# Kernel tuning notes

Hardware: AMD Instinct MI355X
Metric: run time of the kernel (lower is better)

## Reference

```python
import jax, jax.numpy as jnp
import numpy as np

EPS = 1e-5
GROUPS = 32


def _groupnorm(x, gamma, beta):
    B, C, H, W = x.shape
    xr = x.reshape(B, GROUPS, C // GROUPS, H, W)
    mu = xr.mean(axis=(2, 3, 4), keepdims=True)
    var = xr.var(axis=(2, 3, 4), keepdims=True)
    xn = ((xr - mu) * jax.lax.rsqrt(var + EPS)).reshape(B, C, H, W)
    return xn * gamma[None, :, None, None] + beta[None, :, None, None]


def _conv1x1(x, w, b):
    # x: [B,C,H,W], w: [Cout,Cin], b: [Cout]
    return jnp.einsum('bchw,oc->bohw', x, w) + b[None, :, None, None]


def setup_inputs() -> dict:
    key = jax.random.key(0)
    ks = jax.random.split(key, 11)
    B, C, H, W = 4, 64, 64, 64
    s = 0.05  # weight scale for well-conditioned softmax
    inp = {
        'x': jax.random.normal(ks[0], (B, C, H, W), jnp.float32),
        'gn_gamma': jnp.ones((C,), jnp.float32),
        'gn_beta': jnp.zeros((C,), jnp.float32),
        'wq': jax.random.normal(ks[1], (C, C), jnp.float32) * s,
        'bq': jnp.zeros((C,), jnp.float32),
        'wk': jax.random.normal(ks[2], (C, C), jnp.float32) * s,
        'bk': jnp.zeros((C,), jnp.float32),
        'wv': jax.random.normal(ks[3], (C, C), jnp.float32) * s,
        'bv': jnp.zeros((C,), jnp.float32),
        'wp': jax.random.normal(ks[4], (C, C), jnp.float32) * s,
        'bp': jnp.zeros((C,), jnp.float32),
    }
    return inp


def reference(x, gn_gamma, gn_beta, wq, bq, wk, bk, wv, bv, wp, bp):
    B, C, H, W = x.shape
    h = _groupnorm(x, gn_gamma, gn_beta)
    q = _conv1x1(h, wq, bq)
    k = _conv1x1(h, wk, bk)
    v = _conv1x1(h, wv, bv)
    # scores over all spatial positions: [B,H,W,H,W]
    scale = 1.0 / jnp.sqrt(jnp.asarray(C, x.dtype))
    w = jnp.einsum('bchw,bcHW->bhwHW', q, k) * scale
    w = jax.nn.softmax(w.reshape(B, H, W, H * W), axis=-1).reshape(B, H, W, H, W)
    h = jnp.einsum('bhwHW,bcHW->bchw', w, v)
    h = _conv1x1(h, wp, bp)
    return x + h
```

## Files before the change

### kernel.cpp

```cpp
#include <hip/hip_runtime.h>
#include <stdint.h>

#define Bn 4
#define Cn 64
#define Sn 4096
#define Gn 32

typedef float v4f __attribute__((ext_vector_type(4)));
typedef short v8s __attribute__((ext_vector_type(8)));
typedef short v4s __attribute__((ext_vector_type(4)));

#define MFMA16(a,b,c) __builtin_amdgcn_mfma_f32_16x16x32_bf16((a),(b),(c),0,0,0)

__device__ __forceinline__ float bf2f(uint16_t u){
  union { uint32_t i; float f; } x; x.i = ((uint32_t)u) << 16; return x.f;
}
__device__ __forceinline__ uint16_t f2bf(float f){
  union { float f; uint32_t i; } x; x.f = f;
  uint32_t r = x.i + 0x7fffu + ((x.i >> 16) & 1u);
  return (uint16_t)(r >> 16);
}
__device__ __forceinline__ uint16_t f2bf_trunc(float f){
  union { float f; uint32_t i; } x; x.f = f;
  return (uint16_t)(x.i >> 16);
}
__device__ __forceinline__ v8s pack8(float4 a, float4 b){
  v8s r;
  r[0]=(short)f2bf(a.x); r[1]=(short)f2bf(a.y); r[2]=(short)f2bf(a.z); r[3]=(short)f2bf(a.w);
  r[4]=(short)f2bf(b.x); r[5]=(short)f2bf(b.y); r[6]=(short)f2bf(b.z); r[7]=(short)f2bf(b.w);
  return r;
}

__global__ __launch_bounds__(256) void gn_stats(const float* __restrict__ x,
                                                float* __restrict__ stats)
{
  const int tid = threadIdx.x;
  const float* base = x + (size_t)blockIdx.x * 8192;
  float sum = 0.f, sq = 0.f;
  #pragma unroll
  for (int i = 0; i < 8; ++i) {
    float4 v = *(const float4*)(base + ((i << 8) + tid)*4);
    sum += v.x + v.y + v.z + v.w;
    sq  += v.x*v.x + v.y*v.y + v.z*v.z + v.w*v.w;
  }
  #pragma unroll
  for (int off = 1; off < 64; off <<= 1) {
    sum += __shfl_xor(sum, off);
    sq  += __shfl_xor(sq, off);
  }
  __shared__ float red[8];
  const int w = tid >> 6;
  if ((tid & 63) == 0) { red[w] = sum; red[4+w] = sq; }
  __syncthreads();
  if (tid == 0) {
    float s = red[0]+red[1]+red[2]+red[3];
    float q = red[4]+red[5]+red[6]+red[7];
    float mean = s * (1.f/8192.f);
    float var  = q * (1.f/8192.f) - mean*mean;
    stats[blockIdx.x]       = mean;
    stats[128 + blockIdx.x] = rsqrtf(fmaxf(var, 0.f) + 1e-5f);
  }
}

__global__ __launch_bounds__(256) void gn_qkv(
    const float* __restrict__ xg, const float* __restrict__ gamma,
    const float* __restrict__ beta,
    const float* __restrict__ wq, const float* __restrict__ bq,
    const float* __restrict__ wk, const float* __restrict__ bk,
    const float* __restrict__ wv, const float* __restrict__ bv,
    const float* __restrict__ stats,
    uint16_t* __restrict__ Qg, uint16_t* __restrict__ Kg, uint16_t* __restrict__ Vg)
{
  __shared__ uint16_t Hs[16*68];
  const int tid  = threadIdx.x;
  const int w    = tid >> 6;
  const int lane = tid & 63;
  const int l15  = lane & 15;
  const int quad = lane >> 4;
  const int b      = blockIdx.x >> 8;
  const int s_base = (blockIdx.x & 255) << 4;

  {
    const int c = lane;
    const int g = c >> 1;
    const float mean = stats[b*Gn + g];
    const float rstd = stats[128 + b*Gn + g];
    const float ga = gamma[c], be = beta[c];
    float4 v = *(const float4*)(xg + ((size_t)b*Cn + c)*Sn + s_base + (w << 2));
    const int r0 = w << 2;
    Hs[(r0+0)*68 + c] = f2bf((v.x - mean)*rstd*ga + be);
    Hs[(r0+1)*68 + c] = f2bf((v.y - mean)*rstd*ga + be);
    Hs[(r0+2)*68 + c] = f2bf((v.z - mean)*rstd*ga + be);
    Hs[(r0+3)*68 + c] = f2bf((v.w - mean)*rstd*ga + be);
  }
  __syncthreads();

  v8s bh0 = *(const v8s*)(Hs + l15*68 + (quad << 3));
  v8s bh1 = *(const v8s*)(Hs + l15*68 + 32 + (quad << 3));

  #pragma unroll
  for (int t = 0; t < 3; ++t) {
    const int ot   = w*3 + t;
    const int wsel = ot >> 2;
    const int o16  = (ot & 3) << 4;
    const float* Wsel = (wsel == 0) ? wq : (wsel == 1) ? wk : wv;
    const float* Bsel = (wsel == 0) ? bq : (wsel == 1) ? bk : bv;
    const float* Wr = Wsel + (o16 + l15)*64 + (quad << 3);
    v8s a0 = pack8(*(const float4*)(Wr),      *(const float4*)(Wr + 4));
    v8s a1 = pack8(*(const float4*)(Wr + 32), *(const float4*)(Wr + 36));
    v4f d = (v4f){0.f,0.f,0.f,0.f};
    d = MFMA16(a0, bh0, d);
    d = MFMA16(a1, bh1, d);
    const int s = s_base + l15;
    if (wsel <= 1) {
      v4s qv;
      #pragma unroll
      for (int r = 0; r < 4; ++r)
        qv[r] = (short)f2bf(d[r] + Bsel[o16 + (quad << 2) + r]);
      uint16_t* dst = (wsel == 0 ? Qg : Kg) + ((size_t)b*Sn + s)*64 + o16 + (quad << 2);
      *(v4s*)dst = qv;
    } else {
      #pragma unroll
      for (int r = 0; r < 4; ++r) {
        const int o = o16 + (quad << 2) + r;
        Vg[((size_t)b*Cn + o)*Sn + s] = f2bf(d[r] + Bsel[o]);
      }
    }
  }
}

__global__ __launch_bounds__(256) void attn_split(
    const uint16_t* __restrict__ Qg, const uint16_t* __restrict__ Kg,
    const uint16_t* __restrict__ Vg,
    uint16_t* __restrict__ Opart, float* __restrict__ lpart)
{
  __shared__ uint16_t KT[4096];
  __shared__ uint16_t VT[4096];
  __shared__ uint16_t Ps[4][16*68];

  const int tid  = threadIdx.x;
  const int w    = tid >> 6;
  const int lane = tid & 63;
  const int l15  = lane & 15;
  const int quad = lane >> 4;
  const int bx    = blockIdx.x;
  const int split = bx & 3;
  const int qt    = (bx >> 2) & 63;
  const int b     = bx >> 8;
  const int i_base = qt << 6;
  const int j0     = split << 10;

  const uint16_t* Qb = Qg + ((size_t)b*Sn + i_base)*64;
  const uint16_t* Kb = Kg + (size_t)b*Sn*64;
  const uint16_t* Vb = Vg + (size_t)b*Cn*Sn;

  const int arow = (w << 4) + l15;
  v8s aq0 = *(const v8s*)(Qb + (size_t)arow*64 + (quad << 3));
  v8s aq1 = *(const v8s*)(Qb + (size_t)arow*64 + 32 + (quad << 3));

  const int h0 = (tid >> 6) & 1, nA = tid >> 7, nB = nA + 2;
  const int qq = (tid >> 4) & 3, ff = tid & 15;
  const int gcol = h0*32 + qq*8;

  {
    *(v8s*)(KT + (tid << 3))       = *(const v8s*)(Kb + (size_t)(j0 + (nA << 4) + ff)*64 + gcol);
    *(v8s*)(KT + ((tid+256) << 3)) = *(const v8s*)(Kb + (size_t)(j0 + (nB << 4) + ff)*64 + gcol);
    *(v8s*)(VT + (tid << 3))       = *(const v8s*)(Vb + (size_t)((nA << 4) + ff)*Sn + j0 + gcol);
    *(v8s*)(VT + ((tid+256) << 3)) = *(const v8s*)(Vb + (size_t)((nB << 4) + ff)*Sn + j0 + gcol);
  }

  float lsum[4];
  v4f o_acc[4];
  #pragma unroll
  for (int r = 0; r < 4; ++r) { lsum[r] = 0.f; o_acc[r] = (v4f){0.f,0.f,0.f,0.f}; }

  __syncthreads();

  const float SC = 0.18033688011112042f;
  uint16_t* Pw = Ps[w];

  for (int kt = 0; kt < 16; ++kt) {
    v8s kpA, kpB, vpA, vpB;
    if (kt < 15) {
      const int jb = j0 + ((kt + 1) << 6);
      kpA = *(const v8s*)(Kb + (size_t)(jb + (nA << 4) + ff)*64 + gcol);
      kpB = *(const v8s*)(Kb + (size_t)(jb + (nB << 4) + ff)*64 + gcol);
      vpA = *(const v8s*)(Vb + (size_t)((nA << 4) + ff)*Sn + jb + gcol);
      vpB = *(const v8s*)(Vb + (size_t)((nB << 4) + ff)*Sn + jb + gcol);
    }

    v4f s[4];
    #pragma unroll
    for (int n = 0; n < 4; ++n) {
      v8s kb0 = *(const v8s*)(KT + (((n << 1) + 0) << 9) + (lane << 3));
      v8s kb1 = *(const v8s*)(KT + (((n << 1) + 1) << 9) + (lane << 3));
      v4f acc = (v4f){0.f,0.f,0.f,0.f};
      acc = MFMA16(aq0, kb0, acc);
      acc = MFMA16(aq1, kb1, acc);
      s[n] = acc;
    }

    #pragma unroll
    for (int n = 0; n < 4; ++n)
      #pragma unroll
      for (int r = 0; r < 4; ++r) {
        const float pv = __builtin_amdgcn_exp2f(s[n][r]*SC);
        lsum[r] += pv;
        Pw[((quad << 2) + r)*68 + (n << 4) + l15] = f2bf_trunc(pv);
      }

    __asm__ volatile("" ::: "memory");

    v8s ap0 = *(const v8s*)(Pw + l15*68 + (quad << 3));
    v8s ap1 = *(const v8s*)(Pw + l15*68 + 32 + (quad << 3));

    #pragma unroll
    for (int n = 0; n < 4; ++n) {
      v8s vb0 = *(const v8s*)(VT + (((n << 1) + 0) << 9) + (lane << 3));
      v8s vb1 = *(const v8s*)(VT + (((n << 1) + 1) << 9) + (lane << 3));
      v4f o = o_acc[n];
      o = MFMA16(ap0, vb0, o);
      o = MFMA16(ap1, vb1, o);
      o_acc[n] = o;
    }

    __syncthreads();
    if (kt < 15) {
      *(v8s*)(KT + (tid << 3))       = kpA;
      *(v8s*)(KT + ((tid+256) << 3)) = kpB;
      *(v8s*)(VT + (tid << 3))       = vpA;
      *(v8s*)(VT + ((tid+256) << 3)) = vpB;
    }
    __syncthreads();
  }

  #pragma unroll
  for (int r = 0; r < 4; ++r) {
    lsum[r] += __shfl_xor(lsum[r], 1);
    lsum[r] += __shfl_xor(lsum[r], 2);
    lsum[r] += __shfl_xor(lsum[r], 4);
    lsum[r] += __shfl_xor(lsum[r], 8);
  }

  uint16_t* Ob = Opart + (size_t)bx*4096 + (w << 4)*64;
  float*    lp = lpart + bx*64 + (w << 4);
  #pragma unroll
  for (int n = 0; n < 4; ++n)
    #pragma unroll
    for (int r = 0; r < 4; ++r)
      Ob[((quad << 2) + r)*64 + (n << 4) + l15] = f2bf(o_acc[n][r]);
  if (l15 == 0) {
    #pragma unroll
    for (int r = 0; r < 4; ++r) lp[(quad << 2) + r] = lsum[r];
  }
}

__global__ __launch_bounds__(256) void proj_res(
    const uint16_t* __restrict__ Opart, const float* __restrict__ lpart,
    const float* __restrict__ wp, const float* __restrict__ bp,
    const float* __restrict__ xg, float* __restrict__ out)
{
  __shared__ uint16_t As[16*68];
  const int tid  = threadIdx.x;
  const int w    = tid >> 6;
  const int lane = tid & 63;
  const int l15  = lane & 15;
  const int quad = lane >> 4;
  const int b      = blockIdx.x >> 8;
  const int st     = blockIdx.x & 255;
  const int qt     = st >> 2;
  const int sub    = st & 3;
  const int s_base = st << 4;

  const uint16_t* po = Opart + (size_t)((b*64 + qt)*4)*4096 + (sub << 4)*64;
  const float*    pl = lpart + ((b*64 + qt)*4)*64 + (sub << 4);

  {
    const int e = tid << 2, row = tid >> 4, col = (tid & 15) << 2;
    const float linv = 1.f / (pl[row] + pl[64+row] + pl[128+row] + pl[192+row]);
    float acc[4] = {0.f,0.f,0.f,0.f};
    #pragma unroll
    for (int sp = 0; sp < 4; ++sp) {
      v4s o = *(const v4s*)(po + sp*4096 + e);
      #pragma unroll
      for (int j = 0; j < 4; ++j) acc[j] += bf2f((uint16_t)o[j]);
    }
    v4s a;
    #pragma unroll
    for (int j = 0; j < 4; ++j) a[j] = (short)f2bf(acc[j]*linv);
    *(v4s*)(As + row*68 + col) = a;
  }
  __syncthreads();

  v8s ba0 = *(const v8s*)(As + l15*68 + (quad << 3));
  v8s ba1 = *(const v8s*)(As + l15*68 + 32 + (quad << 3));

  const float* Wr = wp + ((w << 4) + l15)*64 + (quad << 3);
  v8s a0 = pack8(*(const float4*)(Wr),      *(const float4*)(Wr + 4));
  v8s a1 = pack8(*(const float4*)(Wr + 32), *(const float4*)(Wr + 36));
  v4f d = (v4f){0.f,0.f,0.f,0.f};
  d = MFMA16(a0, ba0, d);
  d = MFMA16(a1, ba1, d);
  const int s = s_base + l15;
  #pragma unroll
  for (int r = 0; r < 4; ++r) {
    const int o = (w << 4) + (quad << 2) + r;
    const size_t idx = ((size_t)b*Cn + o)*Sn + s;
    out[idx] = d[r] + bp[o] + xg[idx];
  }
}

extern "C" void kernel_launch(void* const* d_in, const int* in_sizes, int n_in,
                              void* d_out, int out_size, void* d_ws, size_t ws_size,
                              hipStream_t stream)
{
  const float* x     = (const float*)d_in[0];
  const float* gamma = (const float*)d_in[1];
  const float* beta  = (const float*)d_in[2];
  const float* wq    = (const float*)d_in[3];
  const float* bq    = (const float*)d_in[4];
  const float* wk    = (const float*)d_in[5];
  const float* bk    = (const float*)d_in[6];
  const float* wv    = (const float*)d_in[7];
  const float* bv    = (const float*)d_in[8];
  const float* wp    = (const float*)d_in[9];
  const float* bp    = (const float*)d_in[10];

  float*    stats = (float*)d_ws;
  uint16_t* Qg    = (uint16_t*)d_ws + 1024;
  uint16_t* Kg    = Qg + (size_t)Bn*Sn*Cn;
  uint16_t* Vg    = Kg + (size_t)Bn*Sn*Cn;
  uint16_t* Opart = Vg + (size_t)Bn*Sn*Cn;
  float*    lpart = (float*)(Opart + (size_t)1024*4096);
  float*    outp  = (float*)d_out;

  gn_stats  <<<128, 256, 0, stream>>>(x, stats);
  gn_qkv    <<<1024, 256, 0, stream>>>(x, gamma, beta, wq, bq, wk, bk, wv, bv,
                                       stats, Qg, Kg, Vg);
  attn_split<<<1024, 256, 0, stream>>>(Qg, Kg, Vg, Opart, lpart);
  proj_res  <<<1024, 256, 0, stream>>>(Opart, lpart, wp, bp, x, outp);
}
```

Baseline: 140.8 us.

## Split attention warps into 2x2 query/key tiles and reuse fragments across tiles

```diff
diff --git a/kernel.cpp b/kernel.cpp
--- a/kernel.cpp
+++ b/kernel.cpp
@@ -136,13 +136,15 @@
 {
   __shared__ uint16_t KT[4096];
   __shared__ uint16_t VT[4096];
-  __shared__ uint16_t Ps[4][16*68];
+  __shared__ uint16_t Ps[4][1280];
 
   const int tid  = threadIdx.x;
   const int w    = tid >> 6;
   const int lane = tid & 63;
   const int l15  = lane & 15;
   const int quad = lane >> 4;
+  const int qh   = w & 1;
+  const int kh   = w >> 1;
   const int bx    = blockIdx.x;
   const int split = bx & 3;
   const int qt    = (bx >> 2) & 63;
@@ -154,25 +156,31 @@
   const uint16_t* Kb = Kg + (size_t)b*Sn*64;
   const uint16_t* Vb = Vg + (size_t)b*Cn*Sn;
 
-  const int arow = (w << 4) + l15;
-  v8s aq0 = *(const v8s*)(Qb + (size_t)arow*64 + (quad << 3));
-  v8s aq1 = *(const v8s*)(Qb + (size_t)arow*64 + 32 + (quad << 3));
-
-  const int h0 = (tid >> 6) & 1, nA = tid >> 7, nB = nA + 2;
-  const int qq = (tid >> 4) & 3, ff = tid & 15;
-  const int gcol = h0*32 + qq*8;
+  v8s qf[2][2];
+  #pragma unroll
+  for (int t = 0; t < 2; ++t) {
+    const uint16_t* qr = Qb + (size_t)((qh << 5) + (t << 4) + l15)*64;
+    qf[t][0] = *(const v8s*)(qr + (quad << 3));
+    qf[t][1] = *(const v8s*)(qr + 32 + (quad << 3));
+  }
+
+  const int s0 = tid, s1 = tid + 256;
+  const int kr0 = ((s0 >> 7) << 4) + (s0 & 15), kc0 = ((s0 >> 6) & 1)*32 + ((s0 >> 4) & 3)*8;
+  const int kr1 = ((s1 >> 7) << 4) + (s1 & 15), kc1 = ((s1 >> 6) & 1)*32 + ((s1 >> 4) & 3)*8;
 
   {
-    *(v8s*)(KT + (tid << 3))       = *(const v8s*)(Kb + (size_t)(j0 + (nA << 4) + ff)*64 + gcol);
-    *(v8s*)(KT + ((tid+256) << 3)) = *(const v8s*)(Kb + (size_t)(j0 + (nB << 4) + ff)*64 + gcol);
-    *(v8s*)(VT + (tid << 3))       = *(const v8s*)(Vb + (size_t)((nA << 4) + ff)*Sn + j0 + gcol);
-    *(v8s*)(VT + ((tid+256) << 3)) = *(const v8s*)(Vb + (size_t)((nB << 4) + ff)*Sn + j0 + gcol);
-  }
-
-  float lsum[4];
-  v4f o_acc[4];
-  #pragma unroll
-  for (int r = 0; r < 4; ++r) { lsum[r] = 0.f; o_acc[r] = (v4f){0.f,0.f,0.f,0.f}; }
+    *(v8s*)(KT + (s0 << 3)) = *(const v8s*)(Kb + (size_t)(j0 + kr0)*64 + kc0);
+    *(v8s*)(KT + (s1 << 3)) = *(const v8s*)(Kb + (size_t)(j0 + kr1)*64 + kc1);
+    *(v8s*)(VT + (s0 << 3)) = *(const v8s*)(Vb + (size_t)kr0*Sn + j0 + kc0);
+    *(v8s*)(VT + (s1 << 3)) = *(const v8s*)(Vb + (size_t)kr1*Sn + j0 + kc1);
+  }
+
+  float lsum[2] = {0.f, 0.f};
+  v4f o_acc[2][4];
+  #pragma unroll
+  for (int t = 0; t < 2; ++t)
+    #pragma unroll
+    for (int n = 0; n < 4; ++n) o_acc[t][n] = (v4f){0.f,0.f,0.f,0.f};
 
   __syncthreads();
 
@@ -183,75 +191,82 @@
     v8s kpA, kpB, vpA, vpB;
     if (kt < 15) {
       const int jb = j0 + ((kt + 1) << 6);
-      kpA = *(const v8s*)(Kb + (size_t)(jb + (nA << 4) + ff)*64 + gcol);
-      kpB = *(const v8s*)(Kb + (size_t)(jb + (nB << 4) + ff)*64 + gcol);
-      vpA = *(const v8s*)(Vb + (size_t)((nA << 4) + ff)*Sn + jb + gcol);
-      vpB = *(const v8s*)(Vb + (size_t)((nB << 4) + ff)*Sn + jb + gcol);
-    }
-
-    v4f s[4];
+      kpA = *(const v8s*)(Kb + (size_t)(jb + kr0)*64 + kc0);
+      kpB = *(const v8s*)(Kb + (size_t)(jb + kr1)*64 + kc1);
+      vpA = *(const v8s*)(Vb + (size_t)kr0*Sn + jb + kc0);
+      vpB = *(const v8s*)(Vb + (size_t)kr1*Sn + jb + kc1);
+    }
+
+    v4f st[2][2];
+    #pragma unroll
+    for (int T = 0; T < 2; ++T) {
+      const int rk = ((kh << 1) + T) << 1;
+      v8s ka0 = *(const v8s*)(KT + ((rk + 0) << 9) + (lane << 3));
+      v8s ka1 = *(const v8s*)(KT + ((rk + 1) << 9) + (lane << 3));
+      #pragma unroll
+      for (int t = 0; t < 2; ++t) {
+        v4f acc = (v4f){0.f,0.f,0.f,0.f};
+        acc = MFMA16(ka0, qf[t][0], acc);
+        acc = MFMA16(ka1, qf[t][1], acc);
+        st[T][t] = acc;
+      }
+    }
+
+    #pragma unroll
+    for (int t = 0; t < 2; ++t)
+      #pragma unroll
+      for (int T = 0; T < 2; ++T) {
+        v4s pw;
+        #pragma unroll
+        for (int r = 0; r < 4; ++r) {
+          const float pv = __builtin_amdgcn_exp2f(st[T][t][r]*SC);
+          lsum[t] += pv;
+          pw[r] = (short)f2bf_trunc(pv);
+        }
+        *(v4s*)(Pw + ((t << 4) + l15)*40 + (T << 4) + (quad << 2)) = pw;
+      }
+
+    __asm__ volatile("" ::: "memory");
+
+    v8s ap[2];
+    #pragma unroll
+    for (int t = 0; t < 2; ++t)
+      ap[t] = *(const v8s*)(Pw + ((t << 4) + l15)*40 + (quad << 3));
+
     #pragma unroll
     for (int n = 0; n < 4; ++n) {
-      v8s kb0 = *(const v8s*)(KT + (((n << 1) + 0) << 9) + (lane << 3));
-      v8s kb1 = *(const v8s*)(KT + (((n << 1) + 1) << 9) + (lane << 3));
-      v4f acc = (v4f){0.f,0.f,0.f,0.f};
-      acc = MFMA16(aq0, kb0, acc);
-      acc = MFMA16(aq1, kb1, acc);
-      s[n] = acc;
-    }
-
-    #pragma unroll
-    for (int n = 0; n < 4; ++n)
-      #pragma unroll
-      for (int r = 0; r < 4; ++r) {
-        const float pv = __builtin_amdgcn_exp2f(s[n][r]*SC);
-        lsum[r] += pv;
-        Pw[((quad << 2) + r)*68 + (n << 4) + l15] = f2bf_trunc(pv);
-      }
-
-    __asm__ volatile("" ::: "memory");
-
-    v8s ap0 = *(const v8s*)(Pw + l15*68 + (quad << 3));
-    v8s ap1 = *(const v8s*)(Pw + l15*68 + 32 + (quad << 3));
-
-    #pragma unroll
-    for (int n = 0; n < 4; ++n) {
-      v8s vb0 = *(const v8s*)(VT + (((n << 1) + 0) << 9) + (lane << 3));
-      v8s vb1 = *(const v8s*)(VT + (((n << 1) + 1) << 9) + (lane << 3));
-      v4f o = o_acc[n];
-      o = MFMA16(ap0, vb0, o);
-      o = MFMA16(ap1, vb1, o);
-      o_acc[n] = o;
+      v8s vb = *(const v8s*)(VT + (((n << 1) + kh) << 9) + (lane << 3));
+      #pragma unroll
+      for (int t = 0; t < 2; ++t)
+        o_acc[t][n] = MFMA16(ap[t], vb, o_acc[t][n]);
     }
 
     __syncthreads();
     if (kt < 15) {
-      *(v8s*)(KT + (tid << 3))       = kpA;
-      *(v8s*)(KT + ((tid+256) << 3)) = kpB;
-      *(v8s*)(VT + (tid << 3))       = vpA;
-      *(v8s*)(VT + ((tid+256) << 3)) = vpB;
+      *(v8s*)(KT + (s0 << 3)) = kpA;
+      *(v8s*)(KT + (s1 << 3)) = kpB;
+      *(v8s*)(VT + (s0 << 3)) = vpA;
+      *(v8s*)(VT + (s1 << 3)) = vpB;
     }
     __syncthreads();
   }
 
   #pragma unroll
-  for (int r = 0; r < 4; ++r) {
-    lsum[r] += __shfl_xor(lsum[r], 1);
-    lsum[r] += __shfl_xor(lsum[r], 2);
-    lsum[r] += __shfl_xor(lsum[r], 4);
-    lsum[r] += __shfl_xor(lsum[r], 8);
-  }
-
-  uint16_t* Ob = Opart + (size_t)bx*4096 + (w << 4)*64;
-  float*    lp = lpart + bx*64 + (w << 4);
-  #pragma unroll
-  for (int n = 0; n < 4; ++n)
-    #pragma unroll
-    for (int r = 0; r < 4; ++r)
-      Ob[((quad << 2) + r)*64 + (n << 4) + l15] = f2bf(o_acc[n][r]);
-  if (l15 == 0) {
-    #pragma unroll
-    for (int r = 0; r < 4; ++r) lp[(quad << 2) + r] = lsum[r];
+  for (int t = 0; t < 2; ++t) {
+    lsum[t] += __shfl_xor(lsum[t], 16);
+    lsum[t] += __shfl_xor(lsum[t], 32);
+  }
+
+  uint16_t* Ob = Opart + ((size_t)bx*2 + kh)*4096;
+  float*    lp = lpart + ((size_t)bx*2 + kh)*64;
+  #pragma unroll
+  for (int t = 0; t < 2; ++t) {
+    #pragma unroll
+    for (int n = 0; n < 4; ++n)
+      #pragma unroll
+      for (int r = 0; r < 4; ++r)
+        Ob[((qh << 5) + (t << 4) + (quad << 2) + r)*64 + (n << 4) + l15] = f2bf(o_acc[t][n][r]);
+    if (quad == 0) lp[(qh << 5) + (t << 4) + l15] = lsum[t];
   }
 }
 
@@ -272,15 +287,18 @@
   const int sub    = st & 3;
   const int s_base = st << 4;
 
-  const uint16_t* po = Opart + (size_t)((b*64 + qt)*4)*4096 + (sub << 4)*64;
-  const float*    pl = lpart + ((b*64 + qt)*4)*64 + (sub << 4);
+  const uint16_t* po = Opart + (size_t)((b*64 + qt)*8)*4096 + (sub << 4)*64;
+  const float*    pl = lpart + ((b*64 + qt)*8)*64 + (sub << 4);
 
   {
     const int e = tid << 2, row = tid >> 4, col = (tid & 15) << 2;
-    const float linv = 1.f / (pl[row] + pl[64+row] + pl[128+row] + pl[192+row]);
+    float lsum = 0.f;
+    #pragma unroll
+    for (int sp = 0; sp < 8; ++sp) lsum += pl[sp*64 + row];
+    const float linv = 1.f / lsum;
     float acc[4] = {0.f,0.f,0.f,0.f};
     #pragma unroll
-    for (int sp = 0; sp < 4; ++sp) {
+    for (int sp = 0; sp < 8; ++sp) {
       v4s o = *(const v4s*)(po + sp*4096 + e);
       #pragma unroll
       for (int j = 0; j < 4; ++j) acc[j] += bf2f((uint16_t)o[j]);
@@ -331,7 +349,7 @@
   uint16_t* Kg    = Qg + (size_t)Bn*Sn*Cn;
   uint16_t* Vg    = Kg + (size_t)Bn*Sn*Cn;
   uint16_t* Opart = Vg + (size_t)Bn*Sn*Cn;
-  float*    lpart = (float*)(Opart + (size_t)1024*4096);
+  float*    lpart = (float*)(Opart + (size_t)2048*4096);
   float*    outp  = (float*)d_out;
 
   gn_stats  <<<128, 256, 0, stream>>>(x, stats);
```

After: 137.6 us. -2.2%, faster.
